# Kernel tuning notes

Measured on AMD Instinct MI355X. Metric: run time of the kernel, lower is better.

Reference implementation:

```python
import jax, jax.numpy as jnp
import numpy as np

EPS = 1e-5

def setup_inputs() -> dict:
    key = jax.random.key(0)
    ks = jax.random.split(key, 8)
    B, Cin, H, W = 16, 64, 512, 64
    Cout = 128  # out_channels == mid_channels (default) == NL1D channels
    return {
        "x": jax.random.normal(ks[0], (B, Cin, H, W), dtype=jnp.float32),
        "conv_w": jax.random.normal(ks[1], (Cout, Cin, 3, 3), dtype=jnp.float32) * 0.05,
        "bn1_g": jnp.ones((Cout,), jnp.float32),
        "bn1_b": jnp.zeros((Cout,), jnp.float32),
        "g_w": jax.random.normal(ks[2], (Cout, Cout), dtype=jnp.float32) * 0.05,
        "g_b": jnp.zeros((Cout,), jnp.float32),
        "out_w": jax.random.normal(ks[3], (Cout, Cout), dtype=jnp.float32) * 0.05,
        "out_b": jnp.zeros((Cout,), jnp.float32),
        "bn2_g": jnp.ones((Cout,), jnp.float32),
        "bn2_b": jnp.zeros((Cout,), jnp.float32),
    }

def _bn_train(x, gamma, beta):
    # BatchNorm2d in training mode: batch stats over (B, H, W) per channel
    mu = jnp.mean(x, axis=(0, 2, 3), keepdims=True)
    var = jnp.mean(jnp.square(x - mu), axis=(0, 2, 3), keepdims=True)
    xn = (x - mu) * jax.lax.rsqrt(var + EPS)
    return xn * gamma[None, :, None, None] + beta[None, :, None, None]

def reference(x, conv_w, bn1_g, bn1_b, g_w, g_b, out_w, out_b, bn2_g, bn2_b):
    # conv: 3x3, reflect padding, no bias -> BN -> ReLU
    xp = jnp.pad(x, ((0, 0), (0, 0), (1, 1), (1, 1)), mode="reflect")
    h = jax.lax.conv_general_dilated(
        xp, conv_w, window_strides=(1, 1), padding="VALID",
        dimension_numbers=("NCHW", "OIHW", "NCHW"))
    h = jax.nn.relu(_bn_train(h, bn1_g, bn1_b))  # [B, C, H, W]

    # NL1D
    B, C, Hh, W = h.shape
    xm = jnp.mean(h, axis=3)  # [B, C, H]
    # layer_norm over (C, H) per batch element, no affine
    mu = jnp.mean(xm, axis=(1, 2), keepdims=True)
    var = jnp.mean(jnp.square(xm - mu), axis=(1, 2), keepdims=True)
    xn = (xm - mu) * jax.lax.rsqrt(var + EPS)

    f = jnp.einsum("bch,bck->bhk", xn, xn) / jnp.sqrt(jnp.float32(C))
    f = jax.nn.softmax(f, axis=2)  # [B, H, H]

    y = jnp.einsum("mc,bch->bmh", g_w, xn) + g_b[None, :, None]  # conv1d 1x1
    y = jnp.einsum("bhk,bmk->bmh", f, y)  # bmm(f, y^T)^T
    y = jnp.einsum("om,bmh->boh", out_w, y) + out_b[None, :, None]  # [B, C, H]

    out = h + y[:, :, :, None]  # broadcast == repeat over W
    return jax.nn.silu(_bn_train(out, bn2_g, bn2_b))
```

## Files before the change

kernel.cpp:

```cpp
#include <hip/hip_runtime.h>
#include <stdint.h>

typedef __attribute__((ext_vector_type(8))) short short8;
typedef __attribute__((ext_vector_type(4))) float f32x4;
typedef __attribute__((ext_vector_type(4))) unsigned int u32x4;

typedef const __attribute__((address_space(1))) unsigned int* gas_u32p;
typedef __attribute__((address_space(3))) unsigned int* las_u32p;

__device__ __forceinline__ unsigned short f2bf(float f){
  union{float f; unsigned u;} v; v.f = f;
  unsigned r = v.u + 0x7FFFu + ((v.u >> 16) & 1u);
  return (unsigned short)(r >> 16);
}
__device__ __forceinline__ void dec8(u32x4 d, float* r){
  union{unsigned a; float f;} t;
  t.a = (d[0] & 0xFFFFu) << 16; r[0]=t.f; t.a = d[0] & 0xFFFF0000u; r[1]=t.f;
  t.a = (d[1] & 0xFFFFu) << 16; r[2]=t.f; t.a = d[1] & 0xFFFF0000u; r[3]=t.f;
  t.a = (d[2] & 0xFFFFu) << 16; r[4]=t.f; t.a = d[2] & 0xFFFF0000u; r[5]=t.f;
  t.a = (d[3] & 0xFFFFu) << 16; r[6]=t.f; t.a = d[3] & 0xFFFF0000u; r[7]=t.f;
}

__global__ __launch_bounds__(256) void k_prep(const float* __restrict__ cw,
                                              unsigned short* __restrict__ wA){
  int i = blockIdx.x*256 + threadIdx.x;
  if(i >= 18*128*32) return;
  int kk = i & 31, m = (i >> 5) & 127, ks = i >> 12;
  int k = ks*32 + kk;
  int pos = k >> 6, cin = k & 63;
  int dh = pos/3, dw = pos - dh*3;
  wA[i] = f2bf(cw[((m*64 + cin)*3 + dh)*3 + dw]);
}

__global__ __launch_bounds__(256) void k_xbf(const float* __restrict__ x,
                                             unsigned short* __restrict__ xbf){
  const int h = blockIdx.x, b = blockIdx.y;
  __shared__ float L[64][65];
  const int t = threadIdx.x;
  #pragma unroll
  for(int i=0;i<4;++i){
    int idx = i*256 + t;
    int c = idx >> 4, w0 = (idx & 15) * 4;
    const float* p = x + (((size_t)b*64 + c)*512 + h)*64 + w0;
    f32x4 v = __builtin_nontemporal_load((const f32x4*)p);
    L[c][w0] = v[0]; L[c][w0+1] = v[1]; L[c][w0+2] = v[2]; L[c][w0+3] = v[3];
  }
  __syncthreads();
  unsigned short* dst = xbf + (((size_t)b*512 + h) << 12);
  #pragma unroll
  for(int i=0;i<8;++i){
    int idx = i*256 + t;
    int w = idx >> 5, c2 = (idx & 31)*2;
    unsigned pk = (unsigned)f2bf(L[c2][w]) | ((unsigned)f2bf(L[c2+1][w]) << 16);
    *(unsigned*)(dst + (w<<6) + c2) = pk;
  }
}

__global__ __launch_bounds__(256, 2) void k_conv(
    const unsigned short* __restrict__ xbf, const unsigned short* __restrict__ wA,
    unsigned short* __restrict__ craw, float* __restrict__ sum_slots,
    float* __restrict__ sq_slots)
{
  const int b = blockIdx.y;
  const int bx = blockIdx.x;
  const int hx = (bx & 7)*16 + (bx >> 3);
  const int h0 = hx * 4;
  __shared__ __align__(16) unsigned short xs[6*4096];
  __shared__ __align__(16) unsigned short wbuf[2][4096];
  __shared__ float red[2][128];
  const int t = threadIdx.x;
  const int lane = t & 63, wv = t >> 6;
  for(int r = wv; r < 6; r += 4){
    int hin = h0 - 1 + r;
    hin = hin < 0 ? 1 : (hin > 511 ? 510 : hin);
    const unsigned short* rsrc = xbf + (((size_t)b*512 + hin) << 12);
    unsigned short* ldsrow = &xs[r*4096];
    #pragma unroll
    for(int it=0; it<8; ++it){
      int o = it*1024 + lane*16;
      int w = o >> 7;
      int q = o & 127;
      int so = (w << 7) + (q ^ (((w >> 1) & 7) << 4));
      __builtin_amdgcn_global_load_lds(
          (gas_u32p)(const void*)((const char*)rsrc + so),
          (las_u32p)(void*)(ldsrow + it*512), 16, 0, 0);
    }
  }
  #pragma unroll
  for(int j=0;j<2;++j){
    int off = j*2048 + wv*512;
    __builtin_amdgcn_global_load_lds(
        (gas_u32p)(const void*)(wA + off + lane*8),
        (las_u32p)(void*)(&wbuf[0][off]), 16, 0, 0);
  }
  const int r15 = lane & 15, quad = lane >> 4;
  int P[4][3];
  #pragma unroll
  for(int nt=0;nt<4;++nt){
    int wn = (nt>>1)*32 + 2*r15 + (nt&1);
    #pragma unroll
    for(int dw=0;dw<3;++dw){
      int wi = wn + dw - 1;
      wi = wi < 0 ? 1 : (wi > 63 ? 62 : wi);
      int s = ((wi >> 1) & 7) << 4;
      P[nt][dw] = (wi << 7) + ((quad*16) ^ (s & 0x30)) + (s & 0x40);
    }
  }
  f32x4 acc[8][4];
  #pragma unroll
  for(int mt=0;mt<8;++mt)
    #pragma unroll
    for(int nt=0;nt<4;++nt){ f32x4 z = {0.f,0.f,0.f,0.f}; acc[mt][nt] = z; }
  __syncthreads();
  const char* xsb = (const char*)xs;
  #pragma unroll
  for(int ks=0; ks<18; ++ks){
    if(ks < 17){
      const unsigned short* wsrc = wA + (ks+1)*4096;
      unsigned short* wdst = &wbuf[(ks+1)&1][0];
      #pragma unroll
      for(int j=0;j<2;++j){
        int off = j*2048 + wv*512;
        __builtin_amdgcn_global_load_lds(
            (gas_u32p)(const void*)(wsrc + off + lane*8),
            (las_u32p)(void*)(wdst + off), 16, 0, 0);
      }
    }
    const int pos = ks >> 1;
    const int dh = pos/3, dw = pos - dh*3;
    const int kbit = (ks & 1) << 6;
    const int rowoff = (wv + dh)*8192;
    const unsigned short* wk = &wbuf[ks&1][0];
    short8 a[8];
    #pragma unroll
    for(int mt=0;mt<8;++mt)
      a[mt] = *(const short8*)(wk + mt*512 + r15*32 + quad*8);
    short8 bfr[4];
    #pragma unroll
    for(int nt=0;nt<4;++nt)
      bfr[nt] = *(const short8*)(xsb + rowoff + (P[nt][dw] ^ kbit));
    __builtin_amdgcn_s_setprio(1);
    #pragma unroll
    for(int mt=0;mt<8;++mt){
      #pragma unroll
      for(int nt=0;nt<4;++nt)
        acc[mt][nt] = __builtin_amdgcn_mfma_f32_16x16x32_bf16(a[mt], bfr[nt], acc[mt][nt], 0,0,0);
    }
    __builtin_amdgcn_s_setprio(0);
    __syncthreads();
  }
  {
    size_t obase = (((size_t)b*128)*512 + (size_t)(h0+wv))*64 + 2*r15;
    #pragma unroll
    for(int mt=0;mt<8;++mt){
      #pragma unroll
      for(int rg=0;rg<4;++rg){
        int co = mt*16 + quad*4 + rg;
        unsigned pk0 = (unsigned)f2bf(acc[mt][0][rg]) | ((unsigned)f2bf(acc[mt][1][rg]) << 16);
        unsigned pk1 = (unsigned)f2bf(acc[mt][2][rg]) | ((unsigned)f2bf(acc[mt][3][rg]) << 16);
        __builtin_nontemporal_store(pk0, (unsigned*)(craw + obase + (size_t)co*32768));
        __builtin_nontemporal_store(pk1, (unsigned*)(craw + obase + (size_t)co*32768 + 32));
      }
    }
  }
  if(t < 128){ red[0][t] = 0.f; red[1][t] = 0.f; }
  __syncthreads();
  #pragma unroll
  for(int mt=0;mt<8;++mt){
    #pragma unroll
    for(int rg=0;rg<4;++rg){
      float s = acc[mt][0][rg] + acc[mt][1][rg] + acc[mt][2][rg] + acc[mt][3][rg];
      float q = acc[mt][0][rg]*acc[mt][0][rg] + acc[mt][1][rg]*acc[mt][1][rg]
              + acc[mt][2][rg]*acc[mt][2][rg] + acc[mt][3][rg]*acc[mt][3][rg];
      #pragma unroll
      for(int m=1;m<16;m<<=1){ s += __shfl_xor(s, m); q += __shfl_xor(q, m); }
      if(r15 == 0){
        int co = mt*16 + quad*4 + rg;
        atomicAdd(&red[0][co], s);
        atomicAdd(&red[1][co], q);
      }
    }
  }
  __syncthreads();
  if(t < 128){
    int slot = bx & 63;
    atomicAdd(&sum_slots[t*64 + slot], red[0][t]);
    atomicAdd(&sq_slots[t*64 + slot], red[1][t]);
  }
}

__device__ __forceinline__ void bn1_coeff(
    const float* sum_slots, const float* sq_slots,
    const float* g1, const float* b1, int c, float* a1, float* c1)
{
  double S = 0.0, Q = 0.0;
  #pragma unroll
  for(int s=0;s<64;++s){ S += (double)sum_slots[c*64+s]; Q += (double)sq_slots[c*64+s]; }
  const double N = 524288.0;
  double mu = S/N, var = Q/N - mu*mu;
  float sc = (float)((double)g1[c] / sqrt(var + 1e-5));
  *a1 = sc;
  *c1 = (float)((double)b1[c] - mu*(double)sc);
}

__global__ __launch_bounds__(256) void k_passB(
    const unsigned short* __restrict__ craw,
    const float* __restrict__ sum_slots, const float* __restrict__ sq_slots,
    const float* __restrict__ g1, const float* __restrict__ b1,
    float* __restrict__ xm,
    float* __restrict__ Sh, float* __restrict__ Qh,
    float* __restrict__ lnS, float* __restrict__ lnQ)
{
  const int c = blockIdx.x, b = blockIdx.y;
  const int t = threadIdx.x, wv = t >> 6, l = t & 63;
  float sc, sf;
  bn1_coeff(sum_slots, sq_slots, g1, b1, c, &sc, &sf);
  const unsigned short* base = craw + (((size_t)b*128 + c)*512)*64;
  float* xrow = xm + ((size_t)b*128 + c)*512;
  float sa = 0.f, qa = 0.f, la = 0.f;
  for(int it=0; it<16; ++it){
    int row = it*32 + wv*8 + (l >> 3);
    int w0 = (l & 7)*8;
    u32x4 d = __builtin_nontemporal_load((const u32x4*)(base + (size_t)row*64 + w0));
    float r[8]; dec8(d, r);
    float tot = 0.f;
    #pragma unroll
    for(int j=0;j<8;++j){
      float v = sc*r[j] + sf;
      v = v > 0.f ? v : 0.f;
      tot += v; sa += v; qa += v*v;
    }
    tot += __shfl_xor(tot, 1); tot += __shfl_xor(tot, 2); tot += __shfl_xor(tot, 4);
    if((l & 7) == 0){
      float mv = tot * (1.f/64.f);
      xrow[row] = mv;
      la += mv*mv;
    }
  }
  #pragma unroll
  for(int m=1;m<64;m<<=1){
    sa += __shfl_xor(sa, m); qa += __shfl_xor(qa, m); la += __shfl_xor(la, m);
  }
  __shared__ float rs[4], rq[4], rl[4];
  if(l == 0){ rs[wv]=sa; rq[wv]=qa; rl[wv]=la; }
  __syncthreads();
  if(t == 0){
    float S = rs[0]+rs[1]+rs[2]+rs[3];
    float Q = rq[0]+rq[1]+rq[2]+rq[3];
    float L = rl[0]+rl[1]+rl[2]+rl[3];
    atomicAdd(&Sh[c], S);
    atomicAdd(&Qh[c], Q);
    atomicAdd(&lnS[b], S * (1.f/64.f));
    atomicAdd(&lnQ[b], L);
  }
}

__device__ __forceinline__ void ln_coeff(const float* lnS, const float* lnQ,
                                         int b, float* mu_o, float* rs_o)
{
  double mu = (double)lnS[b] / 65536.0;
  double var = (double)lnQ[b] / 65536.0 - mu*mu;
  *mu_o = (float)mu;
  *rs_o = (float)(1.0 / sqrt(var + 1e-5));
}

__global__ __launch_bounds__(256) void k_y1(
    const float* __restrict__ xm, const float* __restrict__ lnS,
    const float* __restrict__ lnQ, const float* __restrict__ gw,
    const float* __restrict__ gb, float* __restrict__ y1)
{
  const int kt = blockIdx.x, b = blockIdx.y;
  __shared__ __align__(16) float GT[128*132];
  __shared__ __align__(16) float XN[128*68];
  const int t = threadIdx.x;
  const int k0 = kt*64;
  float mu, rs;
  ln_coeff(lnS, lnQ, b, &mu, &rs);
  #pragma unroll
  for(int i=0;i<16;++i){
    int idx = t + i*256;
    int c4 = (idx & 31)*4, o = idx >> 5;
    float4 v = *(const float4*)&gw[o*128 + c4];
    GT[(c4+0)*132 + o] = v.x; GT[(c4+1)*132 + o] = v.y;
    GT[(c4+2)*132 + o] = v.z; GT[(c4+3)*132 + o] = v.w;
  }
  #pragma unroll
  for(int i=0;i<8;++i){
    int idx = t + i*256;
    int kk4 = (idx & 15)*4, c = idx >> 4;
    float4 v = *(const float4*)&xm[((size_t)b*128 + c)*512 + k0 + kk4];
    XN[c*68 + kk4 + 0] = (v.x - mu)*rs; XN[c*68 + kk4 + 1] = (v.y - mu)*rs;
    XN[c*68 + kk4 + 2] = (v.z - mu)*rs; XN[c*68 + kk4 + 3] = (v.w - mu)*rs;
  }
  __syncthreads();
  const int tx = t & 15, ty = t >> 4;
  float acc[8][4] = {{0}};
  for(int c=0;c<128;++c){
    f32x4 a0 = *(const f32x4*)&GT[c*132 + ty*8];
    f32x4 a1 = *(const f32x4*)&GT[c*132 + ty*8 + 4];
    f32x4 bv = *(const f32x4*)&XN[c*68 + tx*4];
    #pragma unroll
    for(int j=0;j<4;++j){
      #pragma unroll
      for(int i=0;i<4;++i){ acc[i][j] += a0[i]*bv[j]; acc[i+4][j] += a1[i]*bv[j]; }
    }
  }
  #pragma unroll
  for(int i=0;i<8;++i){
    int m = ty*8 + i;
    float bias = gb[m];
    f32x4 o;
    #pragma unroll
    for(int j=0;j<4;++j) o[j] = acc[i][j] + bias;
    *(f32x4*)&y1[((size_t)b*128 + m)*512 + k0 + tx*4] = o;
  }
}

__global__ __launch_bounds__(256) void k_att(
    const float* __restrict__ xm, const float* __restrict__ lnS,
    const float* __restrict__ lnQ, const float* __restrict__ y1,
    const float* __restrict__ ow, const float* __restrict__ obv,
    float* __restrict__ y3,
    float* __restrict__ SyS, float* __restrict__ SyyS, float* __restrict__ SxyS)
{
  const int ht = blockIdx.x, b = blockIdx.y;
  const int h0 = ht*32;
  const int SP = 528;
  __shared__ __align__(16) float S[32*528];
  __shared__ __align__(16) float XH[128*32];
  __shared__ __align__(16) float BUF[8704];
  const int t = threadIdx.x;
  const int tx = t & 15, ty = t >> 4;
  const int lane = t & 63, wv = t >> 6;
  float mu, rs;
  ln_coeff(lnS, lnQ, b, &mu, &rs);
  const float* xb = xm + (size_t)b*128*512;
  #pragma unroll
  for(int i=0;i<4;++i){
    int idx = t + i*256;
    int hh4 = (idx & 7)*4, c = idx >> 3;
    float4 v = *(const float4*)&xb[(size_t)c*512 + h0 + hh4];
    XH[c*32 + hh4 + 0] = (v.x - mu)*rs; XH[c*32 + hh4 + 1] = (v.y - mu)*rs;
    XH[c*32 + hh4 + 2] = (v.z - mu)*rs; XH[c*32 + hh4 + 3] = (v.w - mu)*rs;
  }
  const float sscale = 0.088388347648318447f;
  for(int kt=0;kt<8;++kt){
    int k0 = kt*64;
    #pragma unroll
    for(int i=0;i<8;++i){
      int idx = t + i*256;
      int kk4 = (idx & 15)*4, c = idx >> 4;
      float4 v = *(const float4*)&xb[(size_t)c*512 + k0 + kk4];
      BUF[c*68 + kk4 + 0] = (v.x - mu)*rs; BUF[c*68 + kk4 + 1] = (v.y - mu)*rs;
      BUF[c*68 + kk4 + 2] = (v.z - mu)*rs; BUF[c*68 + kk4 + 3] = (v.w - mu)*rs;
    }
    __syncthreads();
    float acc[2][4] = {{0}};
    for(int c=0;c<128;++c){
      float a0 = XH[c*32 + ty*2];
      float a1 = XH[c*32 + ty*2 + 1];
      f32x4 bv = *(const f32x4*)&BUF[c*68 + tx*4];
      #pragma unroll
      for(int j=0;j<4;++j){ acc[0][j] += a0*bv[j]; acc[1][j] += a1*bv[j]; }
    }
    #pragma unroll
    for(int i=0;i<2;++i){
      f32x4 o;
      #pragma unroll
      for(int j=0;j<4;++j) o[j] = acc[i][j]*sscale;
      *(f32x4*)&S[(ty*2+i)*SP + k0 + tx*4] = o;
    }
    __syncthreads();
  }
  #pragma unroll
  for(int rr=0;rr<8;++rr){
    int row = wv*8 + rr;
    float* rowp = &S[row*SP];
    f32x4 v0 = *(const f32x4*)&rowp[lane*8];
    f32x4 v1 = *(const f32x4*)&rowp[lane*8 + 4];
    float mx = v0[0];
    #pragma unroll
    for(int j=1;j<4;++j) mx = fmaxf(mx, v0[j]);
    #pragma unroll
    for(int j=0;j<4;++j) mx = fmaxf(mx, v1[j]);
    #pragma unroll
    for(int m=1;m<64;m<<=1) mx = fmaxf(mx, __shfl_xor(mx, m));
    float sum = 0.f;
    #pragma unroll
    for(int j=0;j<4;++j){ v0[j] = __expf(v0[j]-mx); sum += v0[j]; }
    #pragma unroll
    for(int j=0;j<4;++j){ v1[j] = __expf(v1[j]-mx); sum += v1[j]; }
    #pragma unroll
    for(int m=1;m<64;m<<=1) sum += __shfl_xor(sum, m);
    float inv = 1.f / sum;
    #pragma unroll
    for(int j=0;j<4;++j){ v0[j] *= inv; v1[j] *= inv; }
    *(f32x4*)&rowp[lane*8] = v0;
    *(f32x4*)&rowp[lane*8+4] = v1;
  }
  __syncthreads();
  float y2a[2][8] = {{0}};
  for(int kt=0;kt<8;++kt){
    int k0 = kt*64;
    #pragma unroll
    for(int i=0;i<8;++i){
      int idx = t + i*256;
      int kk4 = (idx & 15)*4, m = idx >> 4;
      float4 v = *(const float4*)&y1[((size_t)b*128 + m)*512 + k0 + kk4];
      BUF[(kk4+0)*132 + m] = v.x; BUF[(kk4+1)*132 + m] = v.y;
      BUF[(kk4+2)*132 + m] = v.z; BUF[(kk4+3)*132 + m] = v.w;
    }
    __syncthreads();
    for(int kk=0;kk<64;++kk){
      float a0 = S[(ty*2)*SP + k0 + kk];
      float a1 = S[(ty*2+1)*SP + k0 + kk];
      f32x4 b0 = *(const f32x4*)&BUF[kk*132 + tx*8];
      f32x4 b1 = *(const f32x4*)&BUF[kk*132 + tx*8 + 4];
      #pragma unroll
      for(int j=0;j<4;++j){
        y2a[0][j]   += a0*b0[j]; y2a[1][j]   += a1*b0[j];
        y2a[0][j+4] += a0*b1[j]; y2a[1][j+4] += a1*b1[j];
      }
    }
    __syncthreads();
  }
  #pragma unroll
  for(int i=0;i<2;++i)
    #pragma unroll
    for(int j=0;j<8;++j)
      BUF[(ty*2+i)*131 + tx*8 + j] = y2a[i][j];
  float* OWT = S;
  #pragma unroll
  for(int i=0;i<16;++i){
    int idx = t + i*256;
    int m4 = (idx & 31)*4, o = idx >> 5;
    float4 v = *(const float4*)&ow[o*128 + m4];
    OWT[(m4+0)*132 + o] = v.x; OWT[(m4+1)*132 + o] = v.y;
    OWT[(m4+2)*132 + o] = v.z; OWT[(m4+3)*132 + o] = v.w;
  }
  __syncthreads();
  float a2[2][8] = {{0}};
  for(int m=0;m<128;++m){
    f32x4 w0 = *(const f32x4*)&OWT[m*132 + ty*8];
    f32x4 w1 = *(const f32x4*)&OWT[m*132 + ty*8 + 4];
    float h0v = BUF[(tx*2)*131 + m];
    float h1v = BUF[(tx*2+1)*131 + m];
    #pragma unroll
    for(int j=0;j<4;++j){
      a2[0][j]   += w0[j]*h0v; a2[1][j]   += w0[j]*h1v;
      a2[0][j+4] += w1[j]*h0v; a2[1][j+4] += w1[j]*h1v;
    }
  }
  const int slot = ((ht<<4) | b) & 31;
  #pragma unroll
  for(int j=0;j<8;++j){
    int o = ty*8 + j;
    float bias = obv[o];
    float v0 = a2[0][j] + bias;
    float v1 = a2[1][j] + bias;
    size_t off = ((size_t)b*128 + o)*512 + h0 + tx*2;
    float2 st; st.x = v0; st.y = v1;
    *(float2*)&y3[off] = st;
    float2 xv = *(const float2*)&xm[off];
    float sy_ = v0 + v1;
    float syy_ = v0*v0 + v1*v1;
    float sxy_ = v0*xv.x + v1*xv.y;
    #pragma unroll
    for(int m=1;m<16;m<<=1){
      sy_ += __shfl_xor(sy_, m); syy_ += __shfl_xor(syy_, m); sxy_ += __shfl_xor(sxy_, m);
    }
    if(tx == 0){
      atomicAdd(&SyS[o*32 + slot], sy_);
      atomicAdd(&SyyS[o*32 + slot], syy_);
      atomicAdd(&SxyS[o*32 + slot], sxy_);
    }
  }
}

__global__ __launch_bounds__(256) void k_final(
    const unsigned short* __restrict__ craw,
    const float* __restrict__ sum_slots, const float* __restrict__ sq_slots,
    const float* __restrict__ g1, const float* __restrict__ b1,
    const float* __restrict__ Sh, const float* __restrict__ Qh,
    const float* __restrict__ SyS, const float* __restrict__ SyyS,
    const float* __restrict__ SxyS, const float* __restrict__ g2,
    const float* __restrict__ b2, const float* __restrict__ y3,
    float* __restrict__ out)
{
  const int c = blockIdx.x, b = blockIdx.y;
  const int t = threadIdx.x, wv = t >> 6, l = t & 63;
  float a1, c1;
  bn1_coeff(sum_slots, sq_slots, g1, b1, c, &a1, &c1);
  double Sy = 0.0, Syy = 0.0, Sxy = 0.0;
  #pragma unroll
  for(int s=0;s<32;++s){
    Sy  += (double)SyS[c*32+s];
    Syy += (double)SyyS[c*32+s];
    Sxy += (double)SxyS[c*32+s];
  }
  const double N = 524288.0;
  double S2 = (double)Sh[c] + 64.0*Sy;
  double Q2 = (double)Qh[c] + 128.0*Sxy + 64.0*Syy;
  double mu2 = S2/N, var2 = Q2/N - mu2*mu2;
  const float a2 = (float)((double)g2[c] / sqrt(var2 + 1e-5));
  const float c2 = (float)((double)b2[c] - mu2*(double)a2);
  const size_t rb = ((size_t)b*128 + c)*512;
  const unsigned short* base = craw + rb*64;
  const float* yrow = y3 + rb;
  float* ob = out + rb*64;
  for(int it=0; it<16; ++it){
    int row = it*32 + wv*8 + (l >> 3);
    int w0 = (l & 7)*8;
    u32x4 d = __builtin_nontemporal_load((const u32x4*)(base + (size_t)row*64 + w0));
    float yv = yrow[row];
    float r[8]; dec8(d, r);
    f32x4 o0, o1;
    #pragma unroll
    for(int j=0;j<8;++j){
      float h = a1*r[j] + c1; h = h > 0.f ? h : 0.f;
      float z = a2*(h + yv) + c2;
      float val = z * __builtin_amdgcn_rcpf(1.f + __expf(-z));
      if(j < 4) o0[j] = val; else o1[j-4] = val;
    }
    __builtin_nontemporal_store(o0, (f32x4*)(ob + (size_t)row*64 + w0));
    __builtin_nontemporal_store(o1, (f32x4*)(ob + (size_t)row*64 + w0 + 4));
  }
}

extern "C" void kernel_launch(void* const* d_in, const int* in_sizes, int n_in,
                              void* d_out, int out_size, void* d_ws, size_t ws_size,
                              hipStream_t stream)
{
  const float* x      = (const float*)d_in[0];
  const float* conv_w = (const float*)d_in[1];
  const float* bn1_g  = (const float*)d_in[2];
  const float* bn1_b  = (const float*)d_in[3];
  const float* g_w    = (const float*)d_in[4];
  const float* g_b    = (const float*)d_in[5];
  const float* out_w  = (const float*)d_in[6];
  const float* out_b  = (const float*)d_in[7];
  const float* bn2_g  = (const float*)d_in[8];
  const float* bn2_b  = (const float*)d_in[9];
  float* out = (float*)d_out;
  char* ws = (char*)d_ws;

  float* sum_slots = (float*)(ws);
  float* sq_slots  = (float*)(ws + 32768);
  float* SyS       = (float*)(ws + 65536);
  float* SyyS      = (float*)(ws + 81920);
  float* SxyS      = (float*)(ws + 98304);
  float* Sh        = (float*)(ws + 114688);
  float* Qh        = (float*)(ws + 115200);
  float* lnS       = (float*)(ws + 115712);
  float* lnQ       = (float*)(ws + 115776);
  unsigned short* wA = (unsigned short*)(ws + 116224);
  float* y3        = (float*)(ws + 263680);
  unsigned short* craw = (unsigned short*)(ws + 4457984);

  float* xm  = out;
  float* y1  = out + 2*(1u<<20);
  unsigned short* xbf = (unsigned short*)((char*)out + (size_t)64*1024*1024);

  hipMemsetAsync(ws, 0, 115840, stream);
  hipLaunchKernelGGL(k_prep,   dim3(288),      dim3(256), 0, stream, conv_w, wA);
  hipLaunchKernelGGL(k_xbf,    dim3(512,16),   dim3(256), 0, stream, x, xbf);
  hipLaunchKernelGGL(k_conv,   dim3(128,16),   dim3(256), 0, stream, xbf, wA, craw, sum_slots, sq_slots);
  hipLaunchKernelGGL(k_passB,  dim3(128,16),   dim3(256), 0, stream, craw, sum_slots, sq_slots, bn1_g, bn1_b, xm, Sh, Qh, lnS, lnQ);
  hipLaunchKernelGGL(k_y1,     dim3(8,16),     dim3(256), 0, stream, xm, lnS, lnQ, g_w, g_b, y1);
  hipLaunchKernelGGL(k_att,    dim3(16,16),    dim3(256), 0, stream, xm, lnS, lnQ, y1, out_w, out_b, y3, SyS, SyyS, SxyS);
  hipLaunchKernelGGL(k_final,  dim3(128,16),   dim3(256), 0, stream, craw, sum_slots, sq_slots, bn1_g, bn1_b, Sh, Qh, SyS, SyyS, SxyS, bn2_g, bn2_b, y3, out);
}
```

Measured before the change: 694.2 us.

## Store conv output contiguously, drop nontemporal hints, halve attention tile rows

The conv epilogue now maps each lane to four consecutive output columns, so it can write one 8-byte vector instead of two scattered 4-byte nontemporal stores, and the LDS swizzle is adjusted to match. passB and final drop the nontemporal hints on craw loads, which may let the bf16 intermediate stay in cache, and final switches to a flat contiguous 8-byte access pattern. The attention kernel processes 16 query rows per block instead of 32, doubling the grid for more parallelism and staging out_w in chunks to cut LDS use. The smaller tile adds redundant K/V loading per block.

After: 665.7 us. -4.1%, faster.

```diff
diff --git a/kernel.cpp b/kernel.cpp
--- a/kernel.cpp
+++ b/kernel.cpp
@@ -4,6 +4,7 @@
 typedef __attribute__((ext_vector_type(8))) short short8;
 typedef __attribute__((ext_vector_type(4))) float f32x4;
 typedef __attribute__((ext_vector_type(4))) unsigned int u32x4;
+typedef __attribute__((ext_vector_type(2))) unsigned int u32x2;
 
 typedef const __attribute__((address_space(1))) unsigned int* gas_u32p;
 typedef __attribute__((address_space(3))) unsigned int* las_u32p;
@@ -19,6 +20,11 @@
   t.a = (d[1] & 0xFFFFu) << 16; r[2]=t.f; t.a = d[1] & 0xFFFF0000u; r[3]=t.f;
   t.a = (d[2] & 0xFFFFu) << 16; r[4]=t.f; t.a = d[2] & 0xFFFF0000u; r[5]=t.f;
   t.a = (d[3] & 0xFFFFu) << 16; r[6]=t.f; t.a = d[3] & 0xFFFF0000u; r[7]=t.f;
+}
+__device__ __forceinline__ void dec4(u32x2 d, float* r){
+  union{unsigned a; float f;} t;
+  t.a = (d[0] & 0xFFFFu) << 16; r[0]=t.f; t.a = d[0] & 0xFFFF0000u; r[1]=t.f;
+  t.a = (d[1] & 0xFFFFu) << 16; r[2]=t.f; t.a = d[1] & 0xFFFF0000u; r[3]=t.f;
 }
 
 __global__ __launch_bounds__(256) void k_prep(const float* __restrict__ cw,
@@ -80,7 +86,7 @@
       int o = it*1024 + lane*16;
       int w = o >> 7;
       int q = o & 127;
-      int so = (w << 7) + (q ^ (((w >> 1) & 7) << 4));
+      int so = (w << 7) + (q ^ (((w >> 2) & 7) << 4));
       __builtin_amdgcn_global_load_lds(
           (gas_u32p)(const void*)((const char*)rsrc + so),
           (las_u32p)(void*)(ldsrow + it*512), 16, 0, 0);
@@ -97,12 +103,12 @@
   int P[4][3];
   #pragma unroll
   for(int nt=0;nt<4;++nt){
-    int wn = (nt>>1)*32 + 2*r15 + (nt&1);
+    int wn = 4*r15 + nt;
     #pragma unroll
     for(int dw=0;dw<3;++dw){
       int wi = wn + dw - 1;
       wi = wi < 0 ? 1 : (wi > 63 ? 62 : wi);
-      int s = ((wi >> 1) & 7) << 4;
+      int s = ((wi >> 2) & 7) << 4;
       P[nt][dw] = (wi << 7) + ((quad*16) ^ (s & 0x30)) + (s & 0x40);
     }
   }
@@ -150,16 +156,16 @@
     __syncthreads();
   }
   {
-    size_t obase = (((size_t)b*128)*512 + (size_t)(h0+wv))*64 + 2*r15;
+    size_t obase = (((size_t)b*128)*512 + (size_t)(h0+wv))*64 + 4*r15;
     #pragma unroll
     for(int mt=0;mt<8;++mt){
       #pragma unroll
       for(int rg=0;rg<4;++rg){
         int co = mt*16 + quad*4 + rg;
-        unsigned pk0 = (unsigned)f2bf(acc[mt][0][rg]) | ((unsigned)f2bf(acc[mt][1][rg]) << 16);
-        unsigned pk1 = (unsigned)f2bf(acc[mt][2][rg]) | ((unsigned)f2bf(acc[mt][3][rg]) << 16);
-        __builtin_nontemporal_store(pk0, (unsigned*)(craw + obase + (size_t)co*32768));
-        __builtin_nontemporal_store(pk1, (unsigned*)(craw + obase + (size_t)co*32768 + 32));
+        u32x2 pk;
+        pk[0] = (unsigned)f2bf(acc[mt][0][rg]) | ((unsigned)f2bf(acc[mt][1][rg]) << 16);
+        pk[1] = (unsigned)f2bf(acc[mt][2][rg]) | ((unsigned)f2bf(acc[mt][3][rg]) << 16);
+        *(u32x2*)(craw + obase + (size_t)co*32768) = pk;
       }
     }
   }
@@ -221,7 +227,7 @@
   for(int it=0; it<16; ++it){
     int row = it*32 + wv*8 + (l >> 3);
     int w0 = (l & 7)*8;
-    u32x4 d = __builtin_nontemporal_load((const u32x4*)(base + (size_t)row*64 + w0));
+    u32x4 d = *(const u32x4*)(base + (size_t)row*64 + w0);
     float r[8]; dec8(d, r);
     float tot = 0.f;
     #pragma unroll
@@ -324,10 +330,10 @@
     float* __restrict__ SyS, float* __restrict__ SyyS, float* __restrict__ SxyS)
 {
   const int ht = blockIdx.x, b = blockIdx.y;
-  const int h0 = ht*32;
+  const int h0 = ht*16;
   const int SP = 528;
-  __shared__ __align__(16) float S[32*528];
-  __shared__ __align__(16) float XH[128*32];
+  __shared__ __align__(16) float S[16*528];
+  __shared__ __align__(16) float XH[128*16];
   __shared__ __align__(16) float BUF[8704];
   const int t = threadIdx.x;
   const int tx = t & 15, ty = t >> 4;
@@ -336,12 +342,12 @@
   ln_coeff(lnS, lnQ, b, &mu, &rs);
   const float* xb = xm + (size_t)b*128*512;
   #pragma unroll
-  for(int i=0;i<4;++i){
+  for(int i=0;i<2;++i){
     int idx = t + i*256;
-    int hh4 = (idx & 7)*4, c = idx >> 3;
+    int hh4 = (idx & 3)*4, c = idx >> 2;
     float4 v = *(const float4*)&xb[(size_t)c*512 + h0 + hh4];
-    XH[c*32 + hh4 + 0] = (v.x - mu)*rs; XH[c*32 + hh4 + 1] = (v.y - mu)*rs;
-    XH[c*32 + hh4 + 2] = (v.z - mu)*rs; XH[c*32 + hh4 + 3] = (v.w - mu)*rs;
+    XH[c*16 + hh4 + 0] = (v.x - mu)*rs; XH[c*16 + hh4 + 1] = (v.y - mu)*rs;
+    XH[c*16 + hh4 + 2] = (v.z - mu)*rs; XH[c*16 + hh4 + 3] = (v.w - mu)*rs;
   }
   const float sscale = 0.088388347648318447f;
   for(int kt=0;kt<8;++kt){
@@ -355,26 +361,22 @@
       BUF[c*68 + kk4 + 2] = (v.z - mu)*rs; BUF[c*68 + kk4 + 3] = (v.w - mu)*rs;
     }
     __syncthreads();
-    float acc[2][4] = {{0}};
+    float acc[4] = {0,0,0,0};
     for(int c=0;c<128;++c){
-      float a0 = XH[c*32 + ty*2];
-      float a1 = XH[c*32 + ty*2 + 1];
+      float a0 = XH[c*16 + ty];
       f32x4 bv = *(const f32x4*)&BUF[c*68 + tx*4];
       #pragma unroll
-      for(int j=0;j<4;++j){ acc[0][j] += a0*bv[j]; acc[1][j] += a1*bv[j]; }
-    }
-    #pragma unroll
-    for(int i=0;i<2;++i){
-      f32x4 o;
-      #pragma unroll
-      for(int j=0;j<4;++j) o[j] = acc[i][j]*sscale;
-      *(f32x4*)&S[(ty*2+i)*SP + k0 + tx*4] = o;
-    }
-    __syncthreads();
-  }
-  #pragma unroll
-  for(int rr=0;rr<8;++rr){
-    int row = wv*8 + rr;
+      for(int j=0;j<4;++j) acc[j] += a0*bv[j];
+    }
+    f32x4 o;
+    #pragma unroll
+    for(int j=0;j<4;++j) o[j] = acc[j]*sscale;
+    *(f32x4*)&S[ty*SP + k0 + tx*4] = o;
+    __syncthreads();
+  }
+  #pragma unroll
+  for(int rr=0;rr<4;++rr){
+    int row = wv*4 + rr;
     float* rowp = &S[row*SP];
     f32x4 v0 = *(const f32x4*)&rowp[lane*8];
     f32x4 v1 = *(const f32x4*)&rowp[lane*8 + 4];
@@ -399,7 +401,7 @@
     *(f32x4*)&rowp[lane*8+4] = v1;
   }
   __syncthreads();
-  float y2a[2][8] = {{0}};
+  float y2a[8] = {0,0,0,0,0,0,0,0};
   for(int kt=0;kt<8;++kt){
     int k0 = kt*64;
     #pragma unroll
@@ -412,59 +414,49 @@
     }
     __syncthreads();
     for(int kk=0;kk<64;++kk){
-      float a0 = S[(ty*2)*SP + k0 + kk];
-      float a1 = S[(ty*2+1)*SP + k0 + kk];
+      float a0 = S[ty*SP + k0 + kk];
       f32x4 b0 = *(const f32x4*)&BUF[kk*132 + tx*8];
       f32x4 b1 = *(const f32x4*)&BUF[kk*132 + tx*8 + 4];
       #pragma unroll
-      for(int j=0;j<4;++j){
-        y2a[0][j]   += a0*b0[j]; y2a[1][j]   += a1*b0[j];
-        y2a[0][j+4] += a0*b1[j]; y2a[1][j+4] += a1*b1[j];
-      }
-    }
-    __syncthreads();
-  }
-  #pragma unroll
-  for(int i=0;i<2;++i)
-    #pragma unroll
-    for(int j=0;j<8;++j)
-      BUF[(ty*2+i)*131 + tx*8 + j] = y2a[i][j];
+      for(int j=0;j<4;++j){ y2a[j] += a0*b0[j]; y2a[j+4] += a0*b1[j]; }
+    }
+    __syncthreads();
+  }
+  #pragma unroll
+  for(int j=0;j<8;++j)
+    BUF[ty*131 + tx*8 + j] = y2a[j];
   float* OWT = S;
-  #pragma unroll
-  for(int i=0;i<16;++i){
-    int idx = t + i*256;
-    int m4 = (idx & 31)*4, o = idx >> 5;
-    float4 v = *(const float4*)&ow[o*128 + m4];
-    OWT[(m4+0)*132 + o] = v.x; OWT[(m4+1)*132 + o] = v.y;
-    OWT[(m4+2)*132 + o] = v.z; OWT[(m4+3)*132 + o] = v.w;
-  }
-  __syncthreads();
-  float a2[2][8] = {{0}};
-  for(int m=0;m<128;++m){
-    f32x4 w0 = *(const f32x4*)&OWT[m*132 + ty*8];
-    f32x4 w1 = *(const f32x4*)&OWT[m*132 + ty*8 + 4];
-    float h0v = BUF[(tx*2)*131 + m];
-    float h1v = BUF[(tx*2+1)*131 + m];
-    #pragma unroll
-    for(int j=0;j<4;++j){
-      a2[0][j]   += w0[j]*h0v; a2[1][j]   += w0[j]*h1v;
-      a2[0][j+4] += w1[j]*h0v; a2[1][j+4] += w1[j]*h1v;
-    }
+  float a2[8] = {0,0,0,0,0,0,0,0};
+  for(int mc=0;mc<4;++mc){
+    #pragma unroll
+    for(int i=0;i<4;++i){
+      int idx = t + i*256;
+      int o = idx >> 3, m4 = (idx & 7)*4;
+      float4 v = *(const float4*)&ow[o*128 + mc*32 + m4];
+      OWT[(m4+0)*132 + o] = v.x; OWT[(m4+1)*132 + o] = v.y;
+      OWT[(m4+2)*132 + o] = v.z; OWT[(m4+3)*132 + o] = v.w;
+    }
+    __syncthreads();
+    for(int mm=0;mm<32;++mm){
+      f32x4 w0 = *(const f32x4*)&OWT[mm*132 + ty*8];
+      f32x4 w1 = *(const f32x4*)&OWT[mm*132 + ty*8 + 4];
+      float hv = BUF[tx*131 + mc*32 + mm];
+      #pragma unroll
+      for(int j=0;j<4;++j){ a2[j] += w0[j]*hv; a2[j+4] += w1[j]*hv; }
+    }
+    __syncthreads();
   }
   const int slot = ((ht<<4) | b) & 31;
   #pragma unroll
   for(int j=0;j<8;++j){
     int o = ty*8 + j;
-    float bias = obv[o];
-    float v0 = a2[0][j] + bias;
-    float v1 = a2[1][j] + bias;
-    size_t off = ((size_t)b*128 + o)*512 + h0 + tx*2;
-    float2 st; st.x = v0; st.y = v1;
-    *(float2*)&y3[off] = st;
-    float2 xv = *(const float2*)&xm[off];
-    float sy_ = v0 + v1;
-    float syy_ = v0*v0 + v1*v1;
-    float sxy_ = v0*xv.x + v1*xv.y;
+    float v0 = a2[j] + obv[o];
+    size_t off = ((size_t)b*128 + o)*512 + h0 + tx;
+    y3[off] = v0;
+    float xv = xm[off];
+    float sy_ = v0;
+    float syy_ = v0*v0;
+    float sxy_ = v0*xv;
     #pragma unroll
     for(int m=1;m<16;m<<=1){
       sy_ += __shfl_xor(sy_, m); syy_ += __shfl_xor(syy_, m); sxy_ += __shfl_xor(sxy_, m);
@@ -488,7 +480,7 @@
     float* __restrict__ out)
 {
   const int c = blockIdx.x, b = blockIdx.y;
-  const int t = threadIdx.x, wv = t >> 6, l = t & 63;
+  const int t = threadIdx.x;
   float a1, c1;
   bn1_coeff(sum_slots, sq_slots, g1, b1, c, &a1, &c1);
   double Sy = 0.0, Syy = 0.0, Sxy = 0.0;
@@ -509,21 +501,26 @@
   const float* yrow = y3 + rb;
   float* ob = out + rb*64;
   for(int it=0; it<16; ++it){
-    int row = it*32 + wv*8 + (l >> 3);
-    int w0 = (l & 7)*8;
-    u32x4 d = __builtin_nontemporal_load((const u32x4*)(base + (size_t)row*64 + w0));
-    float yv = yrow[row];
-    float r[8]; dec8(d, r);
+    int f0 = it*2048 + t*4;
+    int f1 = f0 + 1024;
+    u32x2 d0 = *(const u32x2*)(base + f0);
+    u32x2 d1 = *(const u32x2*)(base + f1);
+    float yv0 = yrow[f0 >> 6];
+    float yv1 = yrow[f1 >> 6];
+    float r0[4], r1[4];
+    dec4(d0, r0); dec4(d1, r1);
     f32x4 o0, o1;
     #pragma unroll
-    for(int j=0;j<8;++j){
-      float h = a1*r[j] + c1; h = h > 0.f ? h : 0.f;
-      float z = a2*(h + yv) + c2;
-      float val = z * __builtin_amdgcn_rcpf(1.f + __expf(-z));
-      if(j < 4) o0[j] = val; else o1[j-4] = val;
-    }
-    __builtin_nontemporal_store(o0, (f32x4*)(ob + (size_t)row*64 + w0));
-    __builtin_nontemporal_store(o1, (f32x4*)(ob + (size_t)row*64 + w0 + 4));
+    for(int j=0;j<4;++j){
+      float h = a1*r0[j] + c1; h = h > 0.f ? h : 0.f;
+      float z = a2*(h + yv0) + c2;
+      o0[j] = z * __builtin_amdgcn_rcpf(1.f + __expf(-z));
+      float h2 = a1*r1[j] + c1; h2 = h2 > 0.f ? h2 : 0.f;
+      float z2 = a2*(h2 + yv1) + c2;
+      o1[j] = z2 * __builtin_amdgcn_rcpf(1.f + __expf(-z2));
+    }
+    __builtin_nontemporal_store(o0, (f32x4*)(ob + f0));
+    __builtin_nontemporal_store(o1, (f32x4*)(ob + f1));
   }
 }
 
@@ -567,6 +564,6 @@
   hipLaunchKernelGGL(k_conv,   dim3(128,16),   dim3(256), 0, stream, xbf, wA, craw, sum_slots, sq_slots);
   hipLaunchKernelGGL(k_passB,  dim3(128,16),   dim3(256), 0, stream, craw, sum_slots, sq_slots, bn1_g, bn1_b, xm, Sh, Qh, lnS, lnQ);
   hipLaunchKernelGGL(k_y1,     dim3(8,16),     dim3(256), 0, stream, xm, lnS, lnQ, g_w, g_b, y1);
-  hipLaunchKernelGGL(k_att,    dim3(16,16),    dim3(256), 0, stream, xm, lnS, lnQ, y1, out_w, out_b, y3, SyS, SyyS, SxyS);
+  hipLaunchKernelGGL(k_att,    dim3(32,16),    dim3(256), 0, stream, xm, lnS, lnQ, y1, out_w, out_b, y3, SyS, SyyS, SxyS);
   hipLaunchKernelGGL(k_final,  dim3(128,16),   dim3(256), 0, stream, craw, sum_slots, sq_slots, bn1_g, bn1_b, Sh, Qh, SyS, SyyS, SxyS, bn2_g, bn2_b, y3, out);
 }
```
